# Kernel optimization log

Measured on AMD Instinct MI355X. Metric: run time of the kernel, lower is better.

The kernel has to match this reference:

```python
import jax, jax.numpy as jnp
from jax import lax
import numpy as np

B, T, F, H = 512, 256, 128, 256


def setup_inputs() -> dict:
    key = jax.random.key(0)
    ks = jax.random.split(key, 9)
    s = 0.05
    return {
        "X": jax.random.normal(ks[0], (B, T, F), dtype=jnp.float32),
        "attn1_W": jax.random.normal(ks[1], (T + 1, 2 * H + F), dtype=jnp.float32) * s,
        "attn1_b": jax.random.normal(ks[2], (T + 1,), dtype=jnp.float32) * s,
        "attn2_W": jax.random.normal(ks[3], (F, T + 1), dtype=jnp.float32) * s,
        "attn2_b": jax.random.normal(ks[4], (F,), dtype=jnp.float32) * s,
        "W_ih": jax.random.normal(ks[5], (4 * H, F), dtype=jnp.float32) * s,
        "W_hh": jax.random.normal(ks[6], (4 * H, H), dtype=jnp.float32) * s,
        "b_ih": jax.random.normal(ks[7], (4 * H,), dtype=jnp.float32) * s,
        "b_hh": jax.random.normal(ks[8], (4 * H,), dtype=jnp.float32) * s,
    }


def reference(X, attn1_W, attn1_b, attn2_W, attn2_b, W_ih, W_hh, b_ih, b_hh):
    b, t, f = X.shape
    h_dim = W_hh.shape[1]

    def step(carry, x_t):
        h, c = carry
        # input attention: concat [x, h, c] -> tanh(linear) -> linear -> gate x
        z = jnp.concatenate([x_t, h, c], axis=1)  # [B, F+2H]
        a = jnp.tanh(z @ attn1_W.T + attn1_b)      # [B, T+1]
        xi = (a @ attn2_W.T + attn2_b) * x_t       # [B, F]
        # LSTMCell (PyTorch gate order: i, f, g, o)
        gates = xi @ W_ih.T + b_ih + h @ W_hh.T + b_hh  # [B, 4H]
        i_g, f_g, g_g, o_g = jnp.split(gates, 4, axis=1)
        i_g = jax.nn.sigmoid(i_g)
        f_g = jax.nn.sigmoid(f_g)
        g_g = jnp.tanh(g_g)
        o_g = jax.nn.sigmoid(o_g)
        c_new = f_g * c + i_g * g_g
        h_new = o_g * jnp.tanh(c_new)
        return (h_new, c_new), (h_new, c_new)

    h0 = jnp.zeros((b, h_dim), dtype=X.dtype)
    c0 = jnp.zeros((b, h_dim), dtype=X.dtype)
    _, (hs, cs) = lax.scan(step, (h0, c0), jnp.swapaxes(X, 0, 1))  # [T,B,H]
    return jnp.swapaxes(hs, 0, 1), jnp.swapaxes(cs, 0, 1)  # [B,T,H]
```

## Files before the change

kernel.cpp:

```cpp
#include <hip/hip_runtime.h>
#include <hip/hip_bf16.h>


#define Bb 512
#define Tt 256
#define Ff 128
#define Hh 256

#define CH_A1 0
#define CH_A2 25600
#define CH_IH 29824
#define CH_HH 46208
#define CH_TOTAL 78976

typedef unsigned short ushort_t;
typedef ushort_t ushort8 __attribute__((ext_vector_type(8)));

__device__ inline ushort_t f2b_rn(float f) {
    unsigned u = __float_as_uint(f);
    unsigned r = (u + 0x7fffu + ((u >> 16) & 1u)) >> 16;
    return (ushort_t)r;
}
__device__ inline float b2f(ushort_t u) {
    return __uint_as_float(((unsigned)u) << 16);
}

__global__ void conv_kernel(const float* __restrict__ a1,
                            const float* __restrict__ a2,
                            const float* __restrict__ ih,
                            const float* __restrict__ hh,
                            ushort_t* __restrict__ ws) {
    int idx = blockIdx.x * 256 + threadIdx.x;
    if (idx >= CH_TOTAL) return;
    int lane = idx & 63;
    float vals[8];
    if (idx < CH_A2) {
        int rel = idx;
        int nt = rel / (80 * 64);
        int c  = (rel / 64) % 80;
        int j  = nt * 64 + lane;
        #pragma unroll
        for (int e = 0; e < 8; ++e) {
            int k = c * 8 + e;
            vals[e] = (j < 257) ? a1[j * 640 + k] : 0.f;
        }
    } else if (idx < CH_IH) {
        int rel = idx - CH_A2;
        int nt = rel / (33 * 64);
        int c  = (rel / 64) % 33;
        int j  = nt * 64 + lane;
        #pragma unroll
        for (int e = 0; e < 8; ++e) {
            int k = c * 8 + e;
            vals[e] = (k < 257) ? a2[j * 257 + k] : 0.f;
        }
    } else if (idx < CH_HH) {
        int rel = idx - CH_IH;
        int nt = rel / (16 * 64);
        int c  = (rel / 64) % 16;
        int j  = nt * 64 + lane;
        #pragma unroll
        for (int e = 0; e < 8; ++e) vals[e] = ih[j * 128 + c * 8 + e];
    } else {
        int rel = idx - CH_HH;
        int nt = rel / (32 * 64);
        int c  = (rel / 64) % 32;
        int j  = nt * 64 + lane;
        #pragma unroll
        for (int e = 0; e < 8; ++e) vals[e] = hh[j * 256 + c * 8 + e];
    }
    ushort8 o;
    #pragma unroll
    for (int e = 0; e < 8; ++e) o[e] = f2b_rn(vals[e]);
    ((ushort8*)ws)[idx] = o;
}

__global__ __launch_bounds__(512) void lstm_kernel(
    const float* __restrict__ X,
    const float* __restrict__ b1,
    const float* __restrict__ b2,
    const float* __restrict__ bih,
    const float* __restrict__ bhh,
    const ushort_t* __restrict__ wsw,
    float* __restrict__ out)
{
    __shared__ float s_z[2][640];
    __shared__ float s_a[2][264];
    __shared__ float s_xi[2][128];
    __shared__ float s_g[2][1024];

    const int tid  = threadIdx.x;
    const int wave = tid >> 6;
    const int lane = tid & 63;
    const int b0   = blockIdx.x * 2;

    const ushort8* __restrict__ W8 = (const ushort8*)wsw;

    for (int i = tid; i < 2 * 512; i += 512) {
        int r = i >> 9, o = i & 511;
        s_z[r][128 + o] = 0.f;
    }
    if (tid < 14) { int r = tid / 7, o = tid % 7; s_a[r][257 + o] = 0.f; }

    float* __restrict__ hs = out;
    float* __restrict__ cs = out + (size_t)Bb * Tt * Hh;

    for (int t = 0; t < Tt; ++t) {
        __syncthreads();
        if (tid < 256) {
            int r = tid >> 7, f = tid & 127;
            s_z[r][f] = X[((size_t)(b0 + r) * Tt + t) * Ff + f];
        }
        __syncthreads();

        for (int u = wave; u < 10; u += 8) {
            int r = u / 5, jt = u % 5;
            const ushort8* wp = W8 + CH_A1 + (jt * 80) * 64 + lane;
            const float4* sp = (const float4*)&s_z[r][0];
            float a0 = 0.f, a1v = 0.f, a2v = 0.f, a3 = 0.f;
            #pragma unroll 4
            for (int c = 0; c < 80; ++c) {
                ushort8 wv = wp[0]; wp += 64;
                float4 sa = sp[2 * c], sb = sp[2 * c + 1];
                a0 = fmaf(b2f(wv[0]), sa.x, a0);
                a1v = fmaf(b2f(wv[1]), sa.y, a1v);
                a2v = fmaf(b2f(wv[2]), sa.z, a2v);
                a3 = fmaf(b2f(wv[3]), sa.w, a3);
                a0 = fmaf(b2f(wv[4]), sb.x, a0);
                a1v = fmaf(b2f(wv[5]), sb.y, a1v);
                a2v = fmaf(b2f(wv[6]), sb.z, a2v);
                a3 = fmaf(b2f(wv[7]), sb.w, a3);
            }
            float acc = (a0 + a1v) + (a2v + a3);
            int j = jt * 64 + lane;
            if (j < 257) s_a[r][j] = tanhf(acc + b1[j]);
        }
        for (int u = wave; u < 32; u += 8) {
            int r = u >> 4, jt = u & 15;
            const ushort8* wp = W8 + CH_HH + (jt * 32) * 64 + lane;
            const float4* sp = (const float4*)&s_z[r][128];
            float a0 = 0.f, a1v = 0.f, a2v = 0.f, a3 = 0.f;
            #pragma unroll 4
            for (int c = 0; c < 32; ++c) {
                ushort8 wv = wp[0]; wp += 64;
                float4 sa = sp[2 * c], sb = sp[2 * c + 1];
                a0 = fmaf(b2f(wv[0]), sa.x, a0);
                a1v = fmaf(b2f(wv[1]), sa.y, a1v);
                a2v = fmaf(b2f(wv[2]), sa.z, a2v);
                a3 = fmaf(b2f(wv[3]), sa.w, a3);
                a0 = fmaf(b2f(wv[4]), sb.x, a0);
                a1v = fmaf(b2f(wv[5]), sb.y, a1v);
                a2v = fmaf(b2f(wv[6]), sb.z, a2v);
                a3 = fmaf(b2f(wv[7]), sb.w, a3);
            }
            float acc = (a0 + a1v) + (a2v + a3);
            int g = jt * 64 + lane;
            s_g[r][g] = acc + bih[g] + bhh[g];
        }
        __syncthreads();

        for (int u = wave; u < 4; u += 8) {
            int r = u >> 1, jt = u & 1;
            const ushort8* wp = W8 + CH_A2 + (jt * 33) * 64 + lane;
            const float4* sp = (const float4*)&s_a[r][0];
            float a0 = 0.f, a1v = 0.f, a2v = 0.f, a3 = 0.f;
            #pragma unroll 4
            for (int c = 0; c < 33; ++c) {
                ushort8 wv = wp[0]; wp += 64;
                float4 sa = sp[2 * c], sb = sp[2 * c + 1];
                a0 = fmaf(b2f(wv[0]), sa.x, a0);
                a1v = fmaf(b2f(wv[1]), sa.y, a1v);
                a2v = fmaf(b2f(wv[2]), sa.z, a2v);
                a3 = fmaf(b2f(wv[3]), sa.w, a3);
                a0 = fmaf(b2f(wv[4]), sb.x, a0);
                a1v = fmaf(b2f(wv[5]), sb.y, a1v);
                a2v = fmaf(b2f(wv[6]), sb.z, a2v);
                a3 = fmaf(b2f(wv[7]), sb.w, a3);
            }
            float acc = (a0 + a1v) + (a2v + a3);
            int f = jt * 64 + lane;
            s_xi[r][f] = (acc + b2[f]) * s_z[r][f];
        }
        __syncthreads();

        for (int u = wave; u < 32; u += 8) {
            int r = u >> 4, jt = u & 15;
            const ushort8* wp = W8 + CH_IH + (jt * 16) * 64 + lane;
            const float4* sp = (const float4*)&s_xi[r][0];
            float a0 = 0.f, a1v = 0.f, a2v = 0.f, a3 = 0.f;
            #pragma unroll 4
            for (int c = 0; c < 16; ++c) {
                ushort8 wv = wp[0]; wp += 64;
                float4 sa = sp[2 * c], sb = sp[2 * c + 1];
                a0 = fmaf(b2f(wv[0]), sa.x, a0);
                a1v = fmaf(b2f(wv[1]), sa.y, a1v);
                a2v = fmaf(b2f(wv[2]), sa.z, a2v);
                a3 = fmaf(b2f(wv[3]), sa.w, a3);
                a0 = fmaf(b2f(wv[4]), sb.x, a0);
                a1v = fmaf(b2f(wv[5]), sb.y, a1v);
                a2v = fmaf(b2f(wv[6]), sb.z, a2v);
                a3 = fmaf(b2f(wv[7]), sb.w, a3);
            }
            float acc = (a0 + a1v) + (a2v + a3);
            int g = jt * 64 + lane;
            s_g[r][g] += acc;
        }
        __syncthreads();

        {
            int r = tid >> 8, d = tid & 255;
            float gi = s_g[r][d];
            float gf = s_g[r][d + 256];
            float gg = s_g[r][d + 512];
            float go = s_g[r][d + 768];
            float i_g = 1.f / (1.f + expf(-gi));
            float f_g = 1.f / (1.f + expf(-gf));
            float g_g = tanhf(gg);
            float o_g = 1.f / (1.f + expf(-go));
            float c_old = s_z[r][384 + d];
            float c_new = fmaf(f_g, c_old, i_g * g_g);
            float h_new = o_g * tanhf(c_new);
            s_z[r][128 + d] = h_new;
            s_z[r][384 + d] = c_new;
            size_t oidx = ((size_t)(b0 + r) * Tt + t) * Hh + d;
            hs[oidx] = h_new;
            cs[oidx] = c_new;
        }
    }
}

extern "C" void kernel_launch(void* const* d_in, const int* in_sizes, int n_in,
                              void* d_out, int out_size, void* d_ws, size_t ws_size,
                              hipStream_t stream) {
    const float* X   = (const float*)d_in[0];
    const float* a1W = (const float*)d_in[1];
    const float* a1b = (const float*)d_in[2];
    const float* a2W = (const float*)d_in[3];
    const float* a2b = (const float*)d_in[4];
    const float* Wih = (const float*)d_in[5];
    const float* Whh = (const float*)d_in[6];
    const float* bih = (const float*)d_in[7];
    const float* bhh = (const float*)d_in[8];
    ushort_t* ws = (ushort_t*)d_ws;

    hipLaunchKernelGGL(conv_kernel, dim3((CH_TOTAL + 255) / 256), dim3(256), 0, stream,
                       a1W, a2W, Wih, Whh, ws);
    hipLaunchKernelGGL(lstm_kernel, dim3(256), dim3(512), 0, stream,
                       X, a1b, a2b, bih, bhh, ws, (float*)d_out);
}
```

Measured before the change: 6.616 ms.

## Rewrite LSTM recurrence with bf16 MFMA tiles over 16 batch rows per block

Replaces the scalar-FMA matvec kernel with an MFMA-based kernel that processes 16 batch rows per 1024-thread block. The weights are repacked into 16x32 MFMA fragment layout, and activations are stored in LDS as bf16. It also prefetches X for the next step, keeps the cell state in fp32 LDS, and swaps tanhf/expf for fast exp-based approximations. The aim is to raise compute throughput and weight reuse across batch rows. The cost is only 32 blocks on the GPU and extra rounding of h, c and the attention activations to bf16.

```diff
diff --git a/kernel.cpp b/kernel.cpp
--- a/kernel.cpp
+++ b/kernel.cpp
@@ -1,5 +1,4 @@
 #include <hip/hip_runtime.h>
-#include <hip/hip_bf16.h>
 
 
 #define Bb 512
@@ -7,22 +6,40 @@
 #define Ff 128
 #define Hh 256
 
+typedef unsigned short ushort_t;
+typedef short s16x8 __attribute__((ext_vector_type(8)));
+typedef float f32x4 __attribute__((ext_vector_type(4)));
+
+#define A1_NT 17
+#define A1_NK 20
+#define A2_NT 8
+#define A2_NK 9
+#define IH_NT 64
+#define IH_NK 4
+#define HH_NT 64
+#define HH_NK 8
 #define CH_A1 0
-#define CH_A2 25600
-#define CH_IH 29824
-#define CH_HH 46208
-#define CH_TOTAL 78976
-
-typedef unsigned short ushort_t;
-typedef ushort_t ushort8 __attribute__((ext_vector_type(8)));
-
-__device__ inline ushort_t f2b_rn(float f) {
+#define CH_A2 21760
+#define CH_IH 26368
+#define CH_HH 42752
+#define CH_TOTAL 75520
+
+#define ZP 648
+#define AP 296
+#define XIP 136
+#define XP 132
+#define GP 1028
+
+__device__ inline ushort_t f2b(float f) {
     unsigned u = __float_as_uint(f);
     unsigned r = (u + 0x7fffu + ((u >> 16) & 1u)) >> 16;
     return (ushort_t)r;
 }
-__device__ inline float b2f(ushort_t u) {
-    return __uint_as_float(((unsigned)u) << 16);
+__device__ inline float fast_sig(float x) { return 1.f / (1.f + __expf(-x)); }
+__device__ inline float fast_tanh(float x) {
+    float cx = fminf(fmaxf(x, -15.f), 15.f);
+    float e = __expf(2.f * cx);
+    return (e - 1.f) / (e + 1.f);
 }
 
 __global__ void conv_kernel(const float* __restrict__ a1,
@@ -33,49 +50,41 @@
     int idx = blockIdx.x * 256 + threadIdx.x;
     if (idx >= CH_TOTAL) return;
     int lane = idx & 63;
-    float vals[8];
+    int jo = lane & 15;
+    int ko = (lane >> 4) * 8;
+    float v[8];
     if (idx < CH_A2) {
-        int rel = idx;
-        int nt = rel / (80 * 64);
-        int c  = (rel / 64) % 80;
-        int j  = nt * 64 + lane;
-        #pragma unroll
-        for (int e = 0; e < 8; ++e) {
-            int k = c * 8 + e;
-            vals[e] = (j < 257) ? a1[j * 640 + k] : 0.f;
-        }
+        int cix = idx >> 6;
+        int tile = cix / A1_NK, kc = cix % A1_NK;
+        int j = tile * 16 + jo, k = kc * 32 + ko;
+        #pragma unroll
+        for (int e = 0; e < 8; ++e) v[e] = (j < 257) ? a1[j * 640 + k + e] : 0.f;
     } else if (idx < CH_IH) {
-        int rel = idx - CH_A2;
-        int nt = rel / (33 * 64);
-        int c  = (rel / 64) % 33;
-        int j  = nt * 64 + lane;
-        #pragma unroll
-        for (int e = 0; e < 8; ++e) {
-            int k = c * 8 + e;
-            vals[e] = (k < 257) ? a2[j * 257 + k] : 0.f;
-        }
+        int cix = (idx - CH_A2) >> 6;
+        int tile = cix / A2_NK, kc = cix % A2_NK;
+        int j = tile * 16 + jo, k = kc * 32 + ko;
+        #pragma unroll
+        for (int e = 0; e < 8; ++e) v[e] = (k + e < 257) ? a2[j * 257 + k + e] : 0.f;
     } else if (idx < CH_HH) {
-        int rel = idx - CH_IH;
-        int nt = rel / (16 * 64);
-        int c  = (rel / 64) % 16;
-        int j  = nt * 64 + lane;
-        #pragma unroll
-        for (int e = 0; e < 8; ++e) vals[e] = ih[j * 128 + c * 8 + e];
+        int cix = (idx - CH_IH) >> 6;
+        int tile = cix / IH_NK, kc = cix % IH_NK;
+        int j = tile * 16 + jo, k = kc * 32 + ko;
+        #pragma unroll
+        for (int e = 0; e < 8; ++e) v[e] = ih[j * 128 + k + e];
     } else {
-        int rel = idx - CH_HH;
-        int nt = rel / (32 * 64);
-        int c  = (rel / 64) % 32;
-        int j  = nt * 64 + lane;
-        #pragma unroll
-        for (int e = 0; e < 8; ++e) vals[e] = hh[j * 256 + c * 8 + e];
-    }
-    ushort8 o;
+        int cix = (idx - CH_HH) >> 6;
+        int tile = cix / HH_NK, kc = cix % HH_NK;
+        int j = tile * 16 + jo, k = kc * 32 + ko;
+        #pragma unroll
+        for (int e = 0; e < 8; ++e) v[e] = hh[j * 256 + k + e];
+    }
+    union { s16x8 v8; ushort_t u[8]; } o;
     #pragma unroll
-    for (int e = 0; e < 8; ++e) o[e] = f2b_rn(vals[e]);
-    ((ushort8*)ws)[idx] = o;
-}
-
-__global__ __launch_bounds__(512) void lstm_kernel(
+    for (int e = 0; e < 8; ++e) o.u[e] = f2b(v[e]);
+    ((s16x8*)ws)[idx] = o.v8;
+}
+
+__global__ __launch_bounds__(1024) void lstm_mfma(
     const float* __restrict__ X,
     const float* __restrict__ b1,
     const float* __restrict__ b2,
@@ -84,148 +93,179 @@
     const ushort_t* __restrict__ wsw,
     float* __restrict__ out)
 {
-    __shared__ float s_z[2][640];
-    __shared__ float s_a[2][264];
-    __shared__ float s_xi[2][128];
-    __shared__ float s_g[2][1024];
-
-    const int tid  = threadIdx.x;
-    const int wave = tid >> 6;
-    const int lane = tid & 63;
-    const int b0   = blockIdx.x * 2;
-
-    const ushort8* __restrict__ W8 = (const ushort8*)wsw;
-
-    for (int i = tid; i < 2 * 512; i += 512) {
-        int r = i >> 9, o = i & 511;
-        s_z[r][128 + o] = 0.f;
-    }
-    if (tid < 14) { int r = tid / 7, o = tid % 7; s_a[r][257 + o] = 0.f; }
+    __shared__ ushort_t z_bf[16][ZP];
+    __shared__ ushort_t a_bf[16][AP];
+    __shared__ ushort_t xi_bf[16][XIP];
+    __shared__ float    s_x[16][XP];
+    __shared__ float    s_g[16][GP];
+    __shared__ float    s_c[16][256];
+
+    const int tid = threadIdx.x;
+    const int w   = tid >> 6;
+    const int l   = tid & 63;
+    const int lj  = l & 15;
+    const int lr4 = (l >> 4) * 4;
+    const int lk8 = (l >> 4) * 8;
+    const int b0  = blockIdx.x * 16;
+
+    const s16x8* __restrict__ W8 = (const s16x8*)wsw;
+
+    float b1v0 = 0.f, b1v1 = 0.f;
+    { int j = w * 16 + lj; if (j < 257) b1v0 = b1[j]; }
+    if (w == 0) { int j = 256 + lj; if (j < 257) b1v1 = b1[j]; }
+    float b2v = 0.f;
+    if (w >= 8) b2v = b2[(w - 8) * 16 + lj];
+    float bg[4];
+    #pragma unroll
+    for (int i = 0; i < 4; ++i) { int j = (4 * w + i) * 16 + lj; bg[i] = bih[j] + bhh[j]; }
+
+    for (int i = tid; i < 16 * 512; i += 1024) {
+        int r = i >> 9, k = i & 511;
+        z_bf[r][128 + k] = 0;
+    }
+    for (int i = tid; i < 16 * AP; i += 1024) {
+        int r = i / AP, k = i - r * AP;
+        a_bf[r][k] = 0;
+    }
+    for (int i = tid; i < 16 * 256; i += 1024) {
+        int r = i >> 8, d = i & 255;
+        s_c[r][d] = 0.f;
+    }
+    if (tid < 512) {
+        int r = tid >> 5, c4 = (tid & 31) * 4;
+        float4 xv = *(const float4*)&X[((size_t)(b0 + r) * Tt + 0) * Ff + c4];
+        s_x[r][c4] = xv.x; s_x[r][c4 + 1] = xv.y; s_x[r][c4 + 2] = xv.z; s_x[r][c4 + 3] = xv.w;
+        z_bf[r][c4] = f2b(xv.x); z_bf[r][c4 + 1] = f2b(xv.y);
+        z_bf[r][c4 + 2] = f2b(xv.z); z_bf[r][c4 + 3] = f2b(xv.w);
+    }
+    __syncthreads();
 
     float* __restrict__ hs = out;
     float* __restrict__ cs = out + (size_t)Bb * Tt * Hh;
 
+    f32x4 agate[4];
+
     for (int t = 0; t < Tt; ++t) {
-        __syncthreads();
-        if (tid < 256) {
-            int r = tid >> 7, f = tid & 127;
-            s_z[r][f] = X[((size_t)(b0 + r) * Tt + t) * Ff + f];
-        }
-        __syncthreads();
-
-        for (int u = wave; u < 10; u += 8) {
-            int r = u / 5, jt = u % 5;
-            const ushort8* wp = W8 + CH_A1 + (jt * 80) * 64 + lane;
-            const float4* sp = (const float4*)&s_z[r][0];
-            float a0 = 0.f, a1v = 0.f, a2v = 0.f, a3 = 0.f;
+        {
+            f32x4 acc = {0.f, 0.f, 0.f, 0.f};
+            const s16x8* wp = W8 + CH_A1 + (w * A1_NK) * 64 + l;
             #pragma unroll 4
-            for (int c = 0; c < 80; ++c) {
-                ushort8 wv = wp[0]; wp += 64;
-                float4 sa = sp[2 * c], sb = sp[2 * c + 1];
-                a0 = fmaf(b2f(wv[0]), sa.x, a0);
-                a1v = fmaf(b2f(wv[1]), sa.y, a1v);
-                a2v = fmaf(b2f(wv[2]), sa.z, a2v);
-                a3 = fmaf(b2f(wv[3]), sa.w, a3);
-                a0 = fmaf(b2f(wv[4]), sb.x, a0);
-                a1v = fmaf(b2f(wv[5]), sb.y, a1v);
-                a2v = fmaf(b2f(wv[6]), sb.z, a2v);
-                a3 = fmaf(b2f(wv[7]), sb.w, a3);
-            }
-            float acc = (a0 + a1v) + (a2v + a3);
-            int j = jt * 64 + lane;
-            if (j < 257) s_a[r][j] = tanhf(acc + b1[j]);
-        }
-        for (int u = wave; u < 32; u += 8) {
-            int r = u >> 4, jt = u & 15;
-            const ushort8* wp = W8 + CH_HH + (jt * 32) * 64 + lane;
-            const float4* sp = (const float4*)&s_z[r][128];
-            float a0 = 0.f, a1v = 0.f, a2v = 0.f, a3 = 0.f;
+            for (int kc = 0; kc < A1_NK; ++kc) {
+                s16x8 a = *(const s16x8*)&z_bf[lj][kc * 32 + lk8];
+                acc = __builtin_amdgcn_mfma_f32_16x16x32_bf16(a, wp[kc * 64], acc, 0, 0, 0);
+            }
+            int j = w * 16 + lj;
+            if (j < 257) {
+                #pragma unroll
+                for (int q = 0; q < 4; ++q)
+                    a_bf[lr4 + q][j] = f2b(fast_tanh(acc[q] + b1v0));
+            }
+        }
+        if (w == 0) {
+            f32x4 acc = {0.f, 0.f, 0.f, 0.f};
+            const s16x8* wp = W8 + CH_A1 + (16 * A1_NK) * 64 + l;
             #pragma unroll 4
-            for (int c = 0; c < 32; ++c) {
-                ushort8 wv = wp[0]; wp += 64;
-                float4 sa = sp[2 * c], sb = sp[2 * c + 1];
-                a0 = fmaf(b2f(wv[0]), sa.x, a0);
-                a1v = fmaf(b2f(wv[1]), sa.y, a1v);
-                a2v = fmaf(b2f(wv[2]), sa.z, a2v);
-                a3 = fmaf(b2f(wv[3]), sa.w, a3);
-                a0 = fmaf(b2f(wv[4]), sb.x, a0);
-                a1v = fmaf(b2f(wv[5]), sb.y, a1v);
-                a2v = fmaf(b2f(wv[6]), sb.z, a2v);
-                a3 = fmaf(b2f(wv[7]), sb.w, a3);
-            }
-            float acc = (a0 + a1v) + (a2v + a3);
-            int g = jt * 64 + lane;
-            s_g[r][g] = acc + bih[g] + bhh[g];
-        }
-        __syncthreads();
-
-        for (int u = wave; u < 4; u += 8) {
-            int r = u >> 1, jt = u & 1;
-            const ushort8* wp = W8 + CH_A2 + (jt * 33) * 64 + lane;
-            const float4* sp = (const float4*)&s_a[r][0];
-            float a0 = 0.f, a1v = 0.f, a2v = 0.f, a3 = 0.f;
-            #pragma unroll 4
-            for (int c = 0; c < 33; ++c) {
-                ushort8 wv = wp[0]; wp += 64;
-                float4 sa = sp[2 * c], sb = sp[2 * c + 1];
-                a0 = fmaf(b2f(wv[0]), sa.x, a0);
-                a1v = fmaf(b2f(wv[1]), sa.y, a1v);
-                a2v = fmaf(b2f(wv[2]), sa.z, a2v);
-                a3 = fmaf(b2f(wv[3]), sa.w, a3);
-                a0 = fmaf(b2f(wv[4]), sb.x, a0);
-                a1v = fmaf(b2f(wv[5]), sb.y, a1v);
-                a2v = fmaf(b2f(wv[6]), sb.z, a2v);
-                a3 = fmaf(b2f(wv[7]), sb.w, a3);
-            }
-            float acc = (a0 + a1v) + (a2v + a3);
-            int f = jt * 64 + lane;
-            s_xi[r][f] = (acc + b2[f]) * s_z[r][f];
-        }
-        __syncthreads();
-
-        for (int u = wave; u < 32; u += 8) {
-            int r = u >> 4, jt = u & 15;
-            const ushort8* wp = W8 + CH_IH + (jt * 16) * 64 + lane;
-            const float4* sp = (const float4*)&s_xi[r][0];
-            float a0 = 0.f, a1v = 0.f, a2v = 0.f, a3 = 0.f;
-            #pragma unroll 4
-            for (int c = 0; c < 16; ++c) {
-                ushort8 wv = wp[0]; wp += 64;
-                float4 sa = sp[2 * c], sb = sp[2 * c + 1];
-                a0 = fmaf(b2f(wv[0]), sa.x, a0);
-                a1v = fmaf(b2f(wv[1]), sa.y, a1v);
-                a2v = fmaf(b2f(wv[2]), sa.z, a2v);
-                a3 = fmaf(b2f(wv[3]), sa.w, a3);
-                a0 = fmaf(b2f(wv[4]), sb.x, a0);
-                a1v = fmaf(b2f(wv[5]), sb.y, a1v);
-                a2v = fmaf(b2f(wv[6]), sb.z, a2v);
-                a3 = fmaf(b2f(wv[7]), sb.w, a3);
-            }
-            float acc = (a0 + a1v) + (a2v + a3);
-            int g = jt * 64 + lane;
-            s_g[r][g] += acc;
-        }
-        __syncthreads();
-
+            for (int kc = 0; kc < A1_NK; ++kc) {
+                s16x8 a = *(const s16x8*)&z_bf[lj][kc * 32 + lk8];
+                acc = __builtin_amdgcn_mfma_f32_16x16x32_bf16(a, wp[kc * 64], acc, 0, 0, 0);
+            }
+            int j = 256 + lj;
+            if (j < 257) {
+                #pragma unroll
+                for (int q = 0; q < 4; ++q)
+                    a_bf[lr4 + q][j] = f2b(fast_tanh(acc[q] + b1v1));
+            }
+        }
         {
-            int r = tid >> 8, d = tid & 255;
+            s16x8 ah[HH_NK];
+            #pragma unroll
+            for (int kc = 0; kc < HH_NK; ++kc)
+                ah[kc] = *(const s16x8*)&z_bf[lj][128 + kc * 32 + lk8];
+            #pragma unroll
+            for (int i = 0; i < 4; ++i) {
+                f32x4 acc = {0.f, 0.f, 0.f, 0.f};
+                const s16x8* wp = W8 + CH_HH + ((4 * w + i) * HH_NK) * 64 + l;
+                #pragma unroll
+                for (int kc = 0; kc < HH_NK; ++kc)
+                    acc = __builtin_amdgcn_mfma_f32_16x16x32_bf16(ah[kc], wp[kc * 64], acc, 0, 0, 0);
+                agate[i] = acc;
+            }
+        }
+        __syncthreads();
+
+        if (w >= 8) {
+            int p = w - 8;
+            f32x4 acc = {0.f, 0.f, 0.f, 0.f};
+            const s16x8* wp = W8 + CH_A2 + (p * A2_NK) * 64 + l;
+            #pragma unroll 3
+            for (int kc = 0; kc < A2_NK; ++kc) {
+                s16x8 a = *(const s16x8*)&a_bf[lj][kc * 32 + lk8];
+                acc = __builtin_amdgcn_mfma_f32_16x16x32_bf16(a, wp[kc * 64], acc, 0, 0, 0);
+            }
+            int j = p * 16 + lj;
+            #pragma unroll
+            for (int q = 0; q < 4; ++q) {
+                int r = lr4 + q;
+                float xi = (acc[q] + b2v) * s_x[r][j];
+                xi_bf[r][j] = f2b(xi);
+            }
+        }
+        __syncthreads();
+
+        {
+            s16x8 ax[IH_NK];
+            #pragma unroll
+            for (int kc = 0; kc < IH_NK; ++kc)
+                ax[kc] = *(const s16x8*)&xi_bf[lj][kc * 32 + lk8];
+            #pragma unroll
+            for (int i = 0; i < 4; ++i) {
+                f32x4 acc = agate[i];
+                const s16x8* wp = W8 + CH_IH + ((4 * w + i) * IH_NK) * 64 + l;
+                #pragma unroll
+                for (int kc = 0; kc < IH_NK; ++kc)
+                    acc = __builtin_amdgcn_mfma_f32_16x16x32_bf16(ax[kc], wp[kc * 64], acc, 0, 0, 0);
+                int j = (4 * w + i) * 16 + lj;
+                #pragma unroll
+                for (int q = 0; q < 4; ++q)
+                    s_g[lr4 + q][j] = acc[q] + bg[i];
+            }
+        }
+        __syncthreads();
+
+        float4 xv;
+        int xr = 0, xc = 0;
+        bool ldx = (t + 1 < Tt) && (tid < 512);
+        if (ldx) {
+            xr = tid >> 5; xc = (tid & 31) * 4;
+            xv = *(const float4*)&X[((size_t)(b0 + xr) * Tt + (t + 1)) * Ff + xc];
+        }
+        #pragma unroll
+        for (int p4 = 0; p4 < 4; ++p4) {
+            int r = p4 * 4 + (tid >> 8);
+            int d = tid & 255;
             float gi = s_g[r][d];
             float gf = s_g[r][d + 256];
             float gg = s_g[r][d + 512];
             float go = s_g[r][d + 768];
-            float i_g = 1.f / (1.f + expf(-gi));
-            float f_g = 1.f / (1.f + expf(-gf));
-            float g_g = tanhf(gg);
-            float o_g = 1.f / (1.f + expf(-go));
-            float c_old = s_z[r][384 + d];
-            float c_new = fmaf(f_g, c_old, i_g * g_g);
-            float h_new = o_g * tanhf(c_new);
-            s_z[r][128 + d] = h_new;
-            s_z[r][384 + d] = c_new;
-            size_t oidx = ((size_t)(b0 + r) * Tt + t) * Hh + d;
-            hs[oidx] = h_new;
-            cs[oidx] = c_new;
-        }
+            float ig = fast_sig(gi);
+            float fg = fast_sig(gf);
+            float g_g = fast_tanh(gg);
+            float og = fast_sig(go);
+            float cn = fmaf(fg, s_c[r][d], ig * g_g);
+            float hn = og * fast_tanh(cn);
+            s_c[r][d] = cn;
+            z_bf[r][128 + d] = f2b(hn);
+            z_bf[r][384 + d] = f2b(cn);
+            size_t oi = ((size_t)(b0 + r) * Tt + t) * Hh + d;
+            hs[oi] = hn;
+            cs[oi] = cn;
+        }
+        if (ldx) {
+            s_x[xr][xc] = xv.x; s_x[xr][xc + 1] = xv.y; s_x[xr][xc + 2] = xv.z; s_x[xr][xc + 3] = xv.w;
+            z_bf[xr][xc] = f2b(xv.x); z_bf[xr][xc + 1] = f2b(xv.y);
+            z_bf[xr][xc + 2] = f2b(xv.z); z_bf[xr][xc + 3] = f2b(xv.w);
+        }
+        __syncthreads();
     }
 }
 
@@ -243,8 +283,8 @@
     const float* bhh = (const float*)d_in[8];
     ushort_t* ws = (ushort_t*)d_ws;
 
-    hipLaunchKernelGGL(conv_kernel, dim3((CH_TOTAL + 255) / 256), dim3(256), 0, stream,
+    hipLaunchKernelGGL(conv_kernel, dim3(CH_TOTAL / 256), dim3(256), 0, stream,
                        a1W, a2W, Wih, Whh, ws);
-    hipLaunchKernelGGL(lstm_kernel, dim3(256), dim3(512), 0, stream,
+    hipLaunchKernelGGL(lstm_mfma, dim3(32), dim3(1024), 0, stream,
                        X, a1b, a2b, bih, bhh, ws, (float*)d_out);
 }
```

New measurement: 6.474 ms. -2.1%, faster.
